# Performance work log

Measured on AMD Instinct MI355X. Metric: run time of the kernel, lower is better.

Reference implementation:

```python
import jax, jax.numpy as jnp
import numpy as np

N = 100000
E = 1600000
D_IN, D_HID, D_OUT = 64, 64, 64


def setup_inputs() -> dict:
    key = jax.random.key(0)
    ks = jax.random.split(key, 9)
    x = jax.random.normal(ks[0], (N, D_IN), dtype=jnp.float32)
    edge_index = jax.random.randint(ks[1], (2, E), 0, N, dtype=jnp.int64)
    # GCNConv params (glorot-ish scale); bias applied after aggregation (PyG convention)
    W1 = jax.random.normal(ks[2], (D_IN, D_HID), dtype=jnp.float32) / np.sqrt(D_IN)
    b1 = jnp.zeros((D_HID,), dtype=jnp.float32)
    W2 = jax.random.normal(ks[3], (D_HID, D_OUT), dtype=jnp.float32) / np.sqrt(D_HID)
    b2 = jnp.zeros((D_OUT,), dtype=jnp.float32)
    Wout = jax.random.normal(ks[4], (D_OUT, 1), dtype=jnp.float32) / np.sqrt(D_OUT)
    bout = jnp.zeros((1,), dtype=jnp.float32)
    return {"x": x, "edge_index": edge_index, "W1": W1, "b1": b1,
            "W2": W2, "b2": b2, "Wout": Wout, "bout": bout}


def _gcn_conv(h, W, b, src, dst, deg_inv_sqrt):
    # h: [N, d_in]; src/dst: [E+N] (self-loops included); symmetric normalization
    h = h @ W                                   # dense projection [N, d_out]
    norm = deg_inv_sqrt[src] * deg_inv_sqrt[dst]  # [E+N]
    msgs = h[src] * norm[:, None]               # irregular gather [E+N, d_out]
    out = jax.ops.segment_sum(msgs, dst, num_segments=N)  # scatter-add
    return out + b


def reference(x, edge_index, W1, b1, W2, b2, Wout, bout):
    loops = jnp.arange(N, dtype=edge_index.dtype)
    src = jnp.concatenate([edge_index[0], loops])  # source -> target flow
    dst = jnp.concatenate([edge_index[1], loops])
    deg = jax.ops.segment_sum(jnp.ones_like(dst, dtype=x.dtype), dst, num_segments=N)
    deg_inv_sqrt = jnp.where(deg > 0, jax.lax.rsqrt(deg), 0.0)

    h = jax.nn.relu(_gcn_conv(x, W1, b1, src, dst, deg_inv_sqrt))
    h = jax.nn.relu(_gcn_conv(h, W2, b2, src, dst, deg_inv_sqrt))
    return h @ Wout + bout  # [N, 1]
```

## Files before the change

kernel.cpp:

```cpp
#include <hip/hip_runtime.h>

#define NN 100000
#define NE 1600000
#define STRIDE 64
#define NROWG (NN / 4)
#define NBUCK 98
#define BCAP 17408
#define CHUNK 2048
#define NCHUNK ((NE + CHUNK - 1) / CHUNK)

typedef unsigned int uint32;
typedef unsigned short ushort16;

__device__ __forceinline__ float bf2f(ushort16 u) {
    return __uint_as_float(((uint32)u) << 16);
}
__device__ __forceinline__ ushort16 f2bf(float f) {
    uint32 u = __float_as_uint(f);
    u = (u + 0x7FFF + ((u >> 16) & 1)) >> 16;
    return (ushort16)u;
}

__global__ void k_bucketA(const int* __restrict__ src, const int* __restrict__ dst,
                          int* gcur, uint2* __restrict__ stage) {
    __shared__ int lcnt[NBUCK];
    __shared__ int lbase[NBUCK];
    int t = threadIdx.x;
    int e0 = blockIdx.x * CHUNK;
    if (t < NBUCK) lcnt[t] = 0;
    __syncthreads();
    int s[8], d[8], b[8], lp[8];
    int m = 0;
#pragma unroll
    for (int j = 0; j < 8; j++) {
        int e = e0 + j * 256 + t;
        if (e < NE) {
            s[j] = src[e];
            d[j] = dst[e];
            b[j] = d[j] >> 10;
            lp[j] = atomicAdd(&lcnt[b[j]], 1);
            m = j + 1;
        }
    }
    __syncthreads();
    if (t < NBUCK) lbase[t] = atomicAdd(&gcur[t], lcnt[t]);
    __syncthreads();
    for (int j = 0; j < m; j++) {
        int pos = lbase[b[j]] + lp[j];
        if (pos < BCAP) stage[(size_t)b[j] * BCAP + pos] = make_uint2((uint32)s[j], (uint32)d[j]);
    }
}

__global__ __launch_bounds__(512)
void k_buildB(const int* __restrict__ gcur, const uint2* __restrict__ stage,
              int* __restrict__ counts, float* __restrict__ dis, int* __restrict__ csr) {
    __shared__ int lcnt[1024];
    int b = blockIdx.x, t = threadIdx.x;
    for (int i = t; i < 1024; i += 512) lcnt[i] = 0;
    __syncthreads();
    int n = gcur[b]; if (n > BCAP) n = BCAP;
    const uint2* sp = stage + (size_t)b * BCAP;
    for (int i = t; i < n; i += 512) {
        uint2 p = sp[i];
        int dd = (int)p.y;
        int lpos = atomicAdd(&lcnt[dd & 1023], 1);
        if (lpos < STRIDE) csr[(size_t)dd * STRIDE + lpos] = (int)p.x;
    }
    __syncthreads();
    int base = b << 10;
    for (int i = t; i < 1024; i += 512) {
        int r = base + i;
        if (r < NN) {
            int c = lcnt[i];
            counts[r] = c;
            dis[r] = rsqrtf((float)c + 1.0f);
        }
    }
}

__global__ void k_prescale(const float* __restrict__ X, const float* __restrict__ dis,
                           uint32* __restrict__ Xb) {
    int i = blockIdx.x * blockDim.x + threadIdx.x;
    if (i >= NN * 32) return;
    float dd = dis[i >> 5];
    float2 v = ((const float2*)X)[i];
    uint32 a = (uint32)f2bf(v.x * dd);
    uint32 b = (uint32)f2bf(v.y * dd);
    Xb[i] = a | (b << 16);
}

__global__ __launch_bounds__(256, 4)
void k_layer1(const ushort16* __restrict__ Xb, const int* __restrict__ counts,
              const int* __restrict__ csr, const float* __restrict__ dis,
              const float* __restrict__ W1, const float* __restrict__ b1,
              ushort16* __restrict__ Hb) {
    __shared__ __align__(16) float accs[4][64];
    int t = threadIdx.x, lane = t & 63, wid = t >> 6;
    float Wreg[64];
#pragma unroll
    for (int j = 0; j < 64; j++) Wreg[j] = W1[j * 64 + lane];
    float bl = b1[lane];

    for (int g = blockIdx.x; g < NROWG; g += gridDim.x) {
        int row = g * 4 + wid;
        float dr = dis[row];
        float acc = bf2f(Xb[row * 64 + lane]);
        int c = counts[row]; if (c > STRIDE) c = STRIDE;
        const int* cp = csr + (size_t)row * STRIDE;
        int i = 0;
        for (; i + 8 <= c; i += 8) {
            int s0 = cp[i],     s1 = cp[i + 1], s2 = cp[i + 2], s3 = cp[i + 3];
            int s4 = cp[i + 4], s5 = cp[i + 5], s6 = cp[i + 6], s7 = cp[i + 7];
            float f0 = bf2f(Xb[s0 * 64 + lane]);
            float f1 = bf2f(Xb[s1 * 64 + lane]);
            float f2 = bf2f(Xb[s2 * 64 + lane]);
            float f3 = bf2f(Xb[s3 * 64 + lane]);
            float f4 = bf2f(Xb[s4 * 64 + lane]);
            float f5 = bf2f(Xb[s5 * 64 + lane]);
            float f6 = bf2f(Xb[s6 * 64 + lane]);
            float f7 = bf2f(Xb[s7 * 64 + lane]);
            acc += ((f0 + f1) + (f2 + f3)) + ((f4 + f5) + (f6 + f7));
        }
        for (; i + 4 <= c; i += 4) {
            int s0 = cp[i], s1 = cp[i + 1], s2 = cp[i + 2], s3 = cp[i + 3];
            float f0 = bf2f(Xb[s0 * 64 + lane]);
            float f1 = bf2f(Xb[s1 * 64 + lane]);
            float f2 = bf2f(Xb[s2 * 64 + lane]);
            float f3 = bf2f(Xb[s3 * 64 + lane]);
            acc += (f0 + f1) + (f2 + f3);
        }
        for (; i < c; ++i) acc += bf2f(Xb[cp[i] * 64 + lane]);

        accs[wid][lane] = acc;
        float o = 0.f;
#pragma unroll
        for (int k4 = 0; k4 < 16; k4++) {
            float4 q = *reinterpret_cast<const float4*>(&accs[wid][k4 * 4]);
            o = fmaf(q.x, Wreg[k4 * 4 + 0], o);
            o = fmaf(q.y, Wreg[k4 * 4 + 1], o);
            o = fmaf(q.z, Wreg[k4 * 4 + 2], o);
            o = fmaf(q.w, Wreg[k4 * 4 + 3], o);
        }
        float h = fmaxf(fmaf(o, dr, bl), 0.f);
        Hb[row * 64 + lane] = f2bf(h * dr);
    }
}

__global__ __launch_bounds__(256, 4)
void k_layer2(const ushort16* __restrict__ Hb, const int* __restrict__ counts,
              const int* __restrict__ csr, const float* __restrict__ dis,
              const float* __restrict__ W2, const float* __restrict__ b2,
              const float* __restrict__ Wout, const float* __restrict__ bout,
              float* __restrict__ y) {
    __shared__ __align__(16) float accs[4][64];
    int t = threadIdx.x, lane = t & 63, wid = t >> 6;
    float Wreg[64];
#pragma unroll
    for (int j = 0; j < 64; j++) Wreg[j] = W2[j * 64 + lane];
    float bl = b2[lane];
    float wl = Wout[lane];
    float bo = bout[0];

    for (int g = blockIdx.x; g < NROWG; g += gridDim.x) {
        int row = g * 4 + wid;
        float dr = dis[row];
        float acc = bf2f(Hb[row * 64 + lane]);
        int c = counts[row]; if (c > STRIDE) c = STRIDE;
        const int* cp = csr + (size_t)row * STRIDE;
        int i = 0;
        for (; i + 8 <= c; i += 8) {
            int s0 = cp[i],     s1 = cp[i + 1], s2 = cp[i + 2], s3 = cp[i + 3];
            int s4 = cp[i + 4], s5 = cp[i + 5], s6 = cp[i + 6], s7 = cp[i + 7];
            float f0 = bf2f(Hb[s0 * 64 + lane]);
            float f1 = bf2f(Hb[s1 * 64 + lane]);
            float f2 = bf2f(Hb[s2 * 64 + lane]);
            float f3 = bf2f(Hb[s3 * 64 + lane]);
            float f4 = bf2f(Hb[s4 * 64 + lane]);
            float f5 = bf2f(Hb[s5 * 64 + lane]);
            float f6 = bf2f(Hb[s6 * 64 + lane]);
            float f7 = bf2f(Hb[s7 * 64 + lane]);
            acc += ((f0 + f1) + (f2 + f3)) + ((f4 + f5) + (f6 + f7));
        }
        for (; i + 4 <= c; i += 4) {
            int s0 = cp[i], s1 = cp[i + 1], s2 = cp[i + 2], s3 = cp[i + 3];
            float f0 = bf2f(Hb[s0 * 64 + lane]);
            float f1 = bf2f(Hb[s1 * 64 + lane]);
            float f2 = bf2f(Hb[s2 * 64 + lane]);
            float f3 = bf2f(Hb[s3 * 64 + lane]);
            acc += (f0 + f1) + (f2 + f3);
        }
        for (; i < c; ++i) acc += bf2f(Hb[cp[i] * 64 + lane]);

        accs[wid][lane] = acc;
        float o = 0.f;
#pragma unroll
        for (int k4 = 0; k4 < 16; k4++) {
            float4 q = *reinterpret_cast<const float4*>(&accs[wid][k4 * 4]);
            o = fmaf(q.x, Wreg[k4 * 4 + 0], o);
            o = fmaf(q.y, Wreg[k4 * 4 + 1], o);
            o = fmaf(q.z, Wreg[k4 * 4 + 2], o);
            o = fmaf(q.w, Wreg[k4 * 4 + 3], o);
        }
        float v = fmaxf(fmaf(o, dr, bl), 0.f) * wl;
#pragma unroll
        for (int off = 32; off; off >>= 1) v += __shfl_down(v, off);
        if (lane == 0) y[row] = v + bo;
    }
}

extern "C" void kernel_launch(void* const* d_in, const int* in_sizes, int n_in,
                              void* d_out, int out_size, void* d_ws, size_t ws_size,
                              hipStream_t stream) {
    const float* x    = (const float*)d_in[0];
    const int*   ei   = (const int*)d_in[1];
    const int*   src  = ei;
    const int*   dst  = ei + NE;
    const float* W1   = (const float*)d_in[2];
    const float* b1   = (const float*)d_in[3];
    const float* W2   = (const float*)d_in[4];
    const float* b2   = (const float*)d_in[5];
    const float* Wout = (const float*)d_in[6];
    const float* bout = (const float*)d_in[7];
    float* y = (float*)d_out;

    char* ws = (char*)d_ws;
    int*      gcur   = (int*)ws;      ws += 512;
    int*      counts = (int*)ws;      ws += 400128;
    float*    dis    = (float*)ws;    ws += 400128;
    int*      csr    = (int*)ws;      ws += (size_t)NN * STRIDE * 4;
    ushort16* Xb     = (ushort16*)ws; ws += (size_t)NN * 64 * 2;
    ushort16* Hb     = (ushort16*)ws;
    uint2*    stage  = (uint2*)Xb;

    hipMemsetAsync(gcur, 0, NBUCK * sizeof(int), stream);
    k_bucketA<<<NCHUNK, 256, 0, stream>>>(src, dst, gcur, stage);
    k_buildB<<<NBUCK, 512, 0, stream>>>(gcur, stage, counts, dis, csr);
    k_prescale<<<(NN * 32 + 255) / 256, 256, 0, stream>>>(x, dis, (uint32*)Xb);

    k_layer1<<<2048, 256, 0, stream>>>(Xb, counts, csr, dis, W1, b1, Hb);
    k_layer2<<<2048, 256, 0, stream>>>(Hb, counts, csr, dis, W2, b2, Wout, bout, y);
}
```

Baseline: 311.1 us.

## Gather two bf16 features per lane with half-wave edge split; double bucket count

In both layer kernels each lane now loads a packed 32-bit word holding two bf16 features, and the two half-waves process alternate neighbors. The partial sums are combined with a cross-half shuffle, and a zero padding row handles odd neighbor counts. The aim is fewer, wider gather instructions and more edges in flight per wave. Separately, the bucketing pass uses twice as many smaller buckets (512 rows each) to give the CSR-build kernel more blocks. That change shrinks per-bucket capacity, so a heavily skewed destination distribution could overflow a bucket.

```diff
diff --git a/kernel.cpp b/kernel.cpp
--- a/kernel.cpp
+++ b/kernel.cpp
@@ -4,8 +4,8 @@
 #define NE 1600000
 #define STRIDE 64
 #define NROWG (NN / 4)
-#define NBUCK 98
-#define BCAP 17408
+#define NBUCK 196
+#define BCAP 8960
 #define CHUNK 2048
 #define NCHUNK ((NE + CHUNK - 1) / CHUNK)
 
@@ -20,6 +20,8 @@
     u = (u + 0x7FFF + ((u >> 16) & 1)) >> 16;
     return (ushort16)u;
 }
+__device__ __forceinline__ float bflo(uint32 u) { return __uint_as_float(u << 16); }
+__device__ __forceinline__ float bfhi(uint32 u) { return __uint_as_float(u & 0xffff0000u); }
 
 __global__ void k_bucketA(const int* __restrict__ src, const int* __restrict__ dst,
                           int* gcur, uint2* __restrict__ stage) {
@@ -37,7 +39,7 @@
         if (e < NE) {
             s[j] = src[e];
             d[j] = dst[e];
-            b[j] = d[j] >> 10;
+            b[j] = d[j] >> 9;
             lp[j] = atomicAdd(&lcnt[b[j]], 1);
             m = j + 1;
         }
@@ -54,34 +56,35 @@
 __global__ __launch_bounds__(512)
 void k_buildB(const int* __restrict__ gcur, const uint2* __restrict__ stage,
               int* __restrict__ counts, float* __restrict__ dis, int* __restrict__ csr) {
-    __shared__ int lcnt[1024];
+    __shared__ int lcnt[512];
     int b = blockIdx.x, t = threadIdx.x;
-    for (int i = t; i < 1024; i += 512) lcnt[i] = 0;
+    if (t < 512) lcnt[t] = 0;
     __syncthreads();
     int n = gcur[b]; if (n > BCAP) n = BCAP;
     const uint2* sp = stage + (size_t)b * BCAP;
     for (int i = t; i < n; i += 512) {
         uint2 p = sp[i];
         int dd = (int)p.y;
-        int lpos = atomicAdd(&lcnt[dd & 1023], 1);
+        int lpos = atomicAdd(&lcnt[dd & 511], 1);
         if (lpos < STRIDE) csr[(size_t)dd * STRIDE + lpos] = (int)p.x;
     }
     __syncthreads();
-    int base = b << 10;
-    for (int i = t; i < 1024; i += 512) {
-        int r = base + i;
-        if (r < NN) {
-            int c = lcnt[i];
-            counts[r] = c;
-            dis[r] = rsqrtf((float)c + 1.0f);
-        }
+    int base = b << 9;
+    int r = base + t;
+    if (t < 512 && r < NN) {
+        int c = lcnt[t];
+        counts[r] = c;
+        dis[r] = rsqrtf((float)c + 1.0f);
     }
 }
 
 __global__ void k_prescale(const float* __restrict__ X, const float* __restrict__ dis,
-                           uint32* __restrict__ Xb) {
+                           uint32* __restrict__ Xb, uint32* __restrict__ Hbz) {
     int i = blockIdx.x * blockDim.x + threadIdx.x;
-    if (i >= NN * 32) return;
+    if (i >= NN * 32) {
+        if (i < NN * 32 + 32) { Xb[i] = 0u; Hbz[i] = 0u; }
+        return;
+    }
     float dd = dis[i >> 5];
     float2 v = ((const float2*)X)[i];
     uint32 a = (uint32)f2bf(v.x * dd);
@@ -90,48 +93,53 @@
 }
 
 __global__ __launch_bounds__(256, 4)
-void k_layer1(const ushort16* __restrict__ Xb, const int* __restrict__ counts,
+void k_layer1(const uint32* __restrict__ Xb32, const int* __restrict__ counts,
               const int* __restrict__ csr, const float* __restrict__ dis,
               const float* __restrict__ W1, const float* __restrict__ b1,
               ushort16* __restrict__ Hb) {
     __shared__ __align__(16) float accs[4][64];
     int t = threadIdx.x, lane = t & 63, wid = t >> 6;
+    int half = lane >> 5, j = lane & 31;
     float Wreg[64];
 #pragma unroll
-    for (int j = 0; j < 64; j++) Wreg[j] = W1[j * 64 + lane];
+    for (int k = 0; k < 64; k++) Wreg[k] = W1[k * 64 + lane];
     float bl = b1[lane];
 
     for (int g = blockIdx.x; g < NROWG; g += gridDim.x) {
         int row = g * 4 + wid;
         float dr = dis[row];
-        float acc = bf2f(Xb[row * 64 + lane]);
+        uint32 u0 = half ? 0u : Xb32[(size_t)row * 32 + j];
+        float accL = bflo(u0), accH = bfhi(u0);
         int c = counts[row]; if (c > STRIDE) c = STRIDE;
         const int* cp = csr + (size_t)row * STRIDE;
         int i = 0;
-        for (; i + 8 <= c; i += 8) {
-            int s0 = cp[i],     s1 = cp[i + 1], s2 = cp[i + 2], s3 = cp[i + 3];
-            int s4 = cp[i + 4], s5 = cp[i + 5], s6 = cp[i + 6], s7 = cp[i + 7];
-            float f0 = bf2f(Xb[s0 * 64 + lane]);
-            float f1 = bf2f(Xb[s1 * 64 + lane]);
-            float f2 = bf2f(Xb[s2 * 64 + lane]);
-            float f3 = bf2f(Xb[s3 * 64 + lane]);
-            float f4 = bf2f(Xb[s4 * 64 + lane]);
-            float f5 = bf2f(Xb[s5 * 64 + lane]);
-            float f6 = bf2f(Xb[s6 * 64 + lane]);
-            float f7 = bf2f(Xb[s7 * 64 + lane]);
-            acc += ((f0 + f1) + (f2 + f3)) + ((f4 + f5) + (f6 + f7));
-        }
-        for (; i + 4 <= c; i += 4) {
-            int s0 = cp[i], s1 = cp[i + 1], s2 = cp[i + 2], s3 = cp[i + 3];
-            float f0 = bf2f(Xb[s0 * 64 + lane]);
-            float f1 = bf2f(Xb[s1 * 64 + lane]);
-            float f2 = bf2f(Xb[s2 * 64 + lane]);
-            float f3 = bf2f(Xb[s3 * 64 + lane]);
-            acc += (f0 + f1) + (f2 + f3);
-        }
-        for (; i < c; ++i) acc += bf2f(Xb[cp[i] * 64 + lane]);
-
-        accs[wid][lane] = acc;
+        for (; i + 16 <= c; i += 16) {
+#pragma unroll
+            for (int p = 0; p < 8; p++) {
+                int eA = cp[i + 2 * p], eB = cp[i + 2 * p + 1];
+                int s = half ? eB : eA;
+                uint32 u = Xb32[(size_t)s * 32 + j];
+                accL += bflo(u); accH += bfhi(u);
+            }
+        }
+        for (; i + 2 <= c; i += 2) {
+            int eA = cp[i], eB = cp[i + 1];
+            int s = half ? eB : eA;
+            uint32 u = Xb32[(size_t)s * 32 + j];
+            accL += bflo(u); accH += bfhi(u);
+        }
+        if (i < c) {
+            int eA = cp[i];
+            int s = half ? NN : eA;
+            uint32 u = Xb32[(size_t)s * 32 + j];
+            accL += bflo(u); accH += bfhi(u);
+        }
+        accL += __shfl_xor(accL, 32);
+        accH += __shfl_xor(accH, 32);
+        if (lane < 32) {
+            accs[wid][2 * j] = accL;
+            accs[wid][2 * j + 1] = accH;
+        }
         float o = 0.f;
 #pragma unroll
         for (int k4 = 0; k4 < 16; k4++) {
@@ -142,21 +150,22 @@
             o = fmaf(q.w, Wreg[k4 * 4 + 3], o);
         }
         float h = fmaxf(fmaf(o, dr, bl), 0.f);
-        Hb[row * 64 + lane] = f2bf(h * dr);
+        Hb[(size_t)row * 64 + lane] = f2bf(h * dr);
     }
 }
 
 __global__ __launch_bounds__(256, 4)
-void k_layer2(const ushort16* __restrict__ Hb, const int* __restrict__ counts,
+void k_layer2(const uint32* __restrict__ Hb32, const int* __restrict__ counts,
               const int* __restrict__ csr, const float* __restrict__ dis,
               const float* __restrict__ W2, const float* __restrict__ b2,
               const float* __restrict__ Wout, const float* __restrict__ bout,
               float* __restrict__ y) {
     __shared__ __align__(16) float accs[4][64];
     int t = threadIdx.x, lane = t & 63, wid = t >> 6;
+    int half = lane >> 5, j = lane & 31;
     float Wreg[64];
 #pragma unroll
-    for (int j = 0; j < 64; j++) Wreg[j] = W2[j * 64 + lane];
+    for (int k = 0; k < 64; k++) Wreg[k] = W2[k * 64 + lane];
     float bl = b2[lane];
     float wl = Wout[lane];
     float bo = bout[0];
@@ -164,34 +173,38 @@
     for (int g = blockIdx.x; g < NROWG; g += gridDim.x) {
         int row = g * 4 + wid;
         float dr = dis[row];
-        float acc = bf2f(Hb[row * 64 + lane]);
+        uint32 u0 = half ? 0u : Hb32[(size_t)row * 32 + j];
+        float accL = bflo(u0), accH = bfhi(u0);
         int c = counts[row]; if (c > STRIDE) c = STRIDE;
         const int* cp = csr + (size_t)row * STRIDE;
         int i = 0;
-        for (; i + 8 <= c; i += 8) {
-            int s0 = cp[i],     s1 = cp[i + 1], s2 = cp[i + 2], s3 = cp[i + 3];
-            int s4 = cp[i + 4], s5 = cp[i + 5], s6 = cp[i + 6], s7 = cp[i + 7];
-            float f0 = bf2f(Hb[s0 * 64 + lane]);
-            float f1 = bf2f(Hb[s1 * 64 + lane]);
-            float f2 = bf2f(Hb[s2 * 64 + lane]);
-            float f3 = bf2f(Hb[s3 * 64 + lane]);
-            float f4 = bf2f(Hb[s4 * 64 + lane]);
-            float f5 = bf2f(Hb[s5 * 64 + lane]);
-            float f6 = bf2f(Hb[s6 * 64 + lane]);
-            float f7 = bf2f(Hb[s7 * 64 + lane]);
-            acc += ((f0 + f1) + (f2 + f3)) + ((f4 + f5) + (f6 + f7));
-        }
-        for (; i + 4 <= c; i += 4) {
-            int s0 = cp[i], s1 = cp[i + 1], s2 = cp[i + 2], s3 = cp[i + 3];
-            float f0 = bf2f(Hb[s0 * 64 + lane]);
-            float f1 = bf2f(Hb[s1 * 64 + lane]);
-            float f2 = bf2f(Hb[s2 * 64 + lane]);
-            float f3 = bf2f(Hb[s3 * 64 + lane]);
-            acc += (f0 + f1) + (f2 + f3);
-        }
-        for (; i < c; ++i) acc += bf2f(Hb[cp[i] * 64 + lane]);
-
-        accs[wid][lane] = acc;
+        for (; i + 16 <= c; i += 16) {
+#pragma unroll
+            for (int p = 0; p < 8; p++) {
+                int eA = cp[i + 2 * p], eB = cp[i + 2 * p + 1];
+                int s = half ? eB : eA;
+                uint32 u = Hb32[(size_t)s * 32 + j];
+                accL += bflo(u); accH += bfhi(u);
+            }
+        }
+        for (; i + 2 <= c; i += 2) {
+            int eA = cp[i], eB = cp[i + 1];
+            int s = half ? eB : eA;
+            uint32 u = Hb32[(size_t)s * 32 + j];
+            accL += bflo(u); accH += bfhi(u);
+        }
+        if (i < c) {
+            int eA = cp[i];
+            int s = half ? NN : eA;
+            uint32 u = Hb32[(size_t)s * 32 + j];
+            accL += bflo(u); accH += bfhi(u);
+        }
+        accL += __shfl_xor(accL, 32);
+        accH += __shfl_xor(accH, 32);
+        if (lane < 32) {
+            accs[wid][2 * j] = accL;
+            accs[wid][2 * j + 1] = accH;
+        }
         float o = 0.f;
 #pragma unroll
         for (int k4 = 0; k4 < 16; k4++) {
@@ -224,19 +237,19 @@
     float* y = (float*)d_out;
 
     char* ws = (char*)d_ws;
-    int*      gcur   = (int*)ws;      ws += 512;
+    int*      gcur   = (int*)ws;      ws += 1024;
     int*      counts = (int*)ws;      ws += 400128;
     float*    dis    = (float*)ws;    ws += 400128;
     int*      csr    = (int*)ws;      ws += (size_t)NN * STRIDE * 4;
-    ushort16* Xb     = (ushort16*)ws; ws += (size_t)NN * 64 * 2;
+    ushort16* Xb     = (ushort16*)ws; ws += (size_t)(NN + 1) * 64 * 2;
     ushort16* Hb     = (ushort16*)ws;
     uint2*    stage  = (uint2*)Xb;
 
     hipMemsetAsync(gcur, 0, NBUCK * sizeof(int), stream);
     k_bucketA<<<NCHUNK, 256, 0, stream>>>(src, dst, gcur, stage);
     k_buildB<<<NBUCK, 512, 0, stream>>>(gcur, stage, counts, dis, csr);
-    k_prescale<<<(NN * 32 + 255) / 256, 256, 0, stream>>>(x, dis, (uint32*)Xb);
-
-    k_layer1<<<2048, 256, 0, stream>>>(Xb, counts, csr, dis, W1, b1, Hb);
-    k_layer2<<<2048, 256, 0, stream>>>(Hb, counts, csr, dis, W2, b2, Wout, bout, y);
-}
+    k_prescale<<<(NN * 32 + 32 + 255) / 256, 256, 0, stream>>>(x, dis, (uint32*)Xb, (uint32*)Hb);
+
+    k_layer1<<<2048, 256, 0, stream>>>((const uint32*)Xb, counts, csr, dis, W1, b1, Hb);
+    k_layer2<<<2048, 256, 0, stream>>>((const uint32*)Hb, counts, csr, dis, W2, b2, Wout, bout, y);
+}
```

Measured after the change: 341.8 us. 1.1x slower.
